# Kernel tuning notes

Hardware: AMD Instinct MI355X
Metric: run time of the kernel (lower is better)

Reference implementation:

```python
import jax, jax.numpy as jnp
import numpy as np
from jax import lax

# Dimensions (ModelArgs with d_model=1024)
B, L = 2, 1024
D_MODEL = 1024
D_INNER = 2048          # expand * d_model
D_STATE = 16
DT_RANK = 64            # ceil(d_model / 16)
D_CONV = 4


def setup_inputs() -> dict:
    key = jax.random.key(0)
    ks = jax.random.split(key, 8)
    sc = lambda k, shp, s: jax.random.normal(k, shp, dtype=jnp.float32) * s
    x = jax.random.normal(ks[0], (B, L, D_MODEL), dtype=jnp.float32)
    W_in = sc(ks[1], (2 * D_INNER, D_MODEL), 0.02)
    conv_w = sc(ks[2], (D_INNER, D_CONV), 0.2)
    conv_b = jnp.zeros((D_INNER,), jnp.float32)
    W_x = sc(ks[3], (DT_RANK + 2 * D_STATE, D_INNER), 0.02)
    dt_init_std = DT_RANK ** -0.5
    W_dt = jax.random.uniform(ks[4], (D_INNER, DT_RANK), jnp.float32,
                              -dt_init_std, dt_init_std)
    # dt_proj bias: inverse-softplus of dt ~ logUniform(dt_min, dt_max)
    dt_min, dt_max = 1e-3, 1e-1
    u = jax.random.uniform(ks[5], (D_INNER,), jnp.float32)
    dt = jnp.exp(u * (np.log(dt_max) - np.log(dt_min)) + np.log(dt_min))
    dt = jnp.clip(dt, 1e-4, None)
    b_dt = dt + jnp.log(-jnp.expm1(-dt))
    A_log = jnp.log(jnp.tile(jnp.arange(1, D_STATE + 1, dtype=jnp.float32)[None, :],
                             (D_INNER, 1)))
    D = jnp.ones((D_INNER,), jnp.float32)
    W_out = sc(ks[6], (D_MODEL, D_INNER), 0.02)
    return {"x": x, "W_in": W_in, "conv_w": conv_w, "conv_b": conv_b,
            "W_x": W_x, "W_dt": W_dt, "b_dt": b_dt, "A_log": A_log,
            "D": D, "W_out": W_out}


def reference(x, W_in, conv_w, conv_b, W_x, W_dt, b_dt, A_log, D, W_out):
    b, l, _ = x.shape
    d_in, n = A_log.shape
    k = conv_w.shape[1]

    # in_proj, split into conv branch and gating residual
    x_and_res = x @ W_in.T                                 # (b, l, 2*d_in)
    xz, res = jnp.split(x_and_res, [d_in], axis=-1)

    # Causal depthwise conv1d (kernel k, left-pad k-1, truncate to l)
    xp = jnp.pad(xz, ((0, 0), (k - 1, 0), (0, 0)))         # (b, l+k-1, d_in)
    xc = conv_b[None, None, :] + sum(
        xp[:, i:i + l, :] * conv_w[None, None, :, i] for i in range(k))
    xc = jax.nn.silu(xc)                                   # (b, l, d_in)

    # x_proj -> delta, B, C
    x_dbl = xc @ W_x.T                                     # (b, l, dt_rank+2n)
    dlt, Bm, Cm = jnp.split(x_dbl, [DT_RANK, DT_RANK + n], axis=-1)
    delta = jax.nn.softplus(dlt @ W_dt.T + b_dt)           # (b, l, d_in)

    # selective scan
    A = -jnp.exp(A_log)                                    # (d_in, n)
    dA = jnp.exp(delta[..., None] * A[None, None])         # (b, l, d_in, n)
    dBu = (delta * xc)[..., None] * Bm[:, :, None, :]      # (b, l, d_in, n)

    def step(h, inp):
        dA_t, dBu_t, C_t = inp                             # (b,d,n),(b,d,n),(b,n)
        h = dA_t * h + dBu_t
        y = jnp.einsum('bdn,bn->bd', h, C_t)
        return h, y

    h0 = jnp.zeros((b, d_in, n), xc.dtype)
    _, ys = lax.scan(step, h0, (dA.transpose(1, 0, 2, 3),
                                dBu.transpose(1, 0, 2, 3),
                                Cm.transpose(1, 0, 2)))
    y = ys.transpose(1, 0, 2) + xc * D[None, None, :]      # (b, l, d_in)

    y = y * jax.nn.silu(res)
    return y @ W_out.T                                     # (b, l, d_model)
```

## Files before the change

### kernel.cpp

```cpp
#include <hip/hip_runtime.h>
#include <hip/hip_bf16.h>
#include <cmath>

#define DEV __device__ __forceinline__

typedef float  f32x4  __attribute__((ext_vector_type(4)));
typedef __bf16 bf16x8 __attribute__((ext_vector_type(8)));
using u16 = unsigned short;

constexpr int CB   = 2;
constexpr int CLEN = 1024;
constexpr int CDM  = 1024;
constexpr int CDI  = 2048;
constexpr int CM   = CB * CLEN;
constexpr int NCHUNK = 64;
constexpr int CHL    = 16;

DEV u16 f2bf(float f) {
  unsigned u = __builtin_bit_cast(unsigned, f);
  unsigned r = (u + 0x7fffu + ((u >> 16) & 1u)) >> 16;
  return (u16)r;
}
DEV float bf2f(u16 v) { return __builtin_bit_cast(float, ((unsigned)v) << 16); }

DEV ushort4 f4bf(float4 v) {
  ushort4 o;
  o.x = f2bf(v.x); o.y = f2bf(v.y); o.z = f2bf(v.z); o.w = f2bf(v.w);
  return o;
}

constexpr int CG_X   = 524288;
constexpr int CG_WIN = CG_X   + 1048576;
constexpr int CG_WDT = CG_WIN + 32768;
constexpr int CG_WO  = CG_WDT + 524288;
constexpr int CG_WX  = CG_WO  + 65536;

__global__ void cast_all_k(const float* __restrict__ x, const float* __restrict__ W_in,
                           const float* __restrict__ W_dt, const float* __restrict__ W_out,
                           const float* __restrict__ W_x,
                           u16* __restrict__ xb, u16* __restrict__ W_inb,
                           u16* __restrict__ W_dtb, u16* __restrict__ W_outb,
                           u16* __restrict__ W_xb)
{
  int i = blockIdx.x * blockDim.x + threadIdx.x;
  if (i < CG_X) {
    reinterpret_cast<ushort4*>(xb)[i] = f4bf(reinterpret_cast<const float4*>(x)[i]);
  } else if (i < CG_WIN) {
    int j = i - CG_X;
    reinterpret_cast<ushort4*>(W_inb)[j] = f4bf(reinterpret_cast<const float4*>(W_in)[j]);
  } else if (i < CG_WDT) {
    int j = i - CG_WIN;
    reinterpret_cast<ushort4*>(W_dtb)[j] = f4bf(reinterpret_cast<const float4*>(W_dt)[j]);
  } else if (i < CG_WO) {
    int j = i - CG_WDT;
    reinterpret_cast<ushort4*>(W_outb)[j] = f4bf(reinterpret_cast<const float4*>(W_out)[j]);
  } else {
    int j = i - CG_WO;
    int base = j * 4, row = base >> 11, col = base & 2047;
    float4 v = make_float4(0.f, 0.f, 0.f, 0.f);
    if (row < 96) v = *reinterpret_cast<const float4*>(W_x + row * 2048 + col);
    reinterpret_cast<ushort4*>(W_xb)[j] = f4bf(v);
  }
}

DEV void gload_lds16(const void* g, void* l) {
  __builtin_amdgcn_global_load_lds(
      (const __attribute__((address_space(1))) void*)g,
      (__attribute__((address_space(3))) void*)l, 16, 0, 0);
}

template <int EPI, int SPLITK>
__global__ __launch_bounds__(256, 2)
void gemm_bt(const u16* __restrict__ A, const u16* __restrict__ Bw,
             float* __restrict__ C, u16* __restrict__ Cb,
             const float* __restrict__ bias,
             int Nd, int Kd, int lda, int ldb, int ldc, size_t slice_stride)
{
  __shared__ u16 As[128 * 32];
  __shared__ u16 Bs[128 * 32];
  const int tid  = threadIdx.x;
  const int wave = tid >> 6;
  const int lane = tid & 63;
  const int wm = wave >> 1, wn = wave & 1;
  const int row0 = blockIdx.y * 128;
  const int col0 = blockIdx.x * 128;
  const int lr = lane >> 2;
  const int lc = (lane & 3) * 8;

  const int kper = Kd / SPLITK;
  const int kbeg = (SPLITK > 1) ? blockIdx.z * kper : 0;
  float* Cz = (SPLITK > 1) ? C + (size_t)blockIdx.z * slice_stride : C;

  f32x4 acc[4][4] = {};

  for (int k0 = kbeg; k0 < kbeg + kper; k0 += 32) {
#pragma unroll
    for (int j = 0; j < 2; ++j) {
      const int rb = j * 64 + wave * 16;
      gload_lds16(A  + (size_t)(row0 + rb + lr) * lda + k0 + lc, As + rb * 32);
      gload_lds16(Bw + (size_t)(col0 + rb + lr) * ldb + k0 + lc, Bs + rb * 32);
    }
    __syncthreads();

    const int q  = lane >> 4;
    const int mr = lane & 15;
    bf16x8 af[4], bfr[4];
#pragma unroll
    for (int t = 0; t < 4; ++t) {
      af[t]  = *reinterpret_cast<const bf16x8*>(As + (wm * 64 + t * 16 + mr) * 32 + q * 8);
      bfr[t] = *reinterpret_cast<const bf16x8*>(Bs + (wn * 64 + t * 16 + mr) * 32 + q * 8);
    }
#pragma unroll
    for (int mt = 0; mt < 4; ++mt)
#pragma unroll
      for (int nt = 0; nt < 4; ++nt)
        acc[mt][nt] = __builtin_amdgcn_mfma_f32_16x16x32_bf16(af[mt], bfr[nt], acc[mt][nt], 0, 0, 0);
    __syncthreads();
  }

  const int q  = lane >> 4;
  const int cn = lane & 15;
#pragma unroll
  for (int mt = 0; mt < 4; ++mt)
#pragma unroll
    for (int nt = 0; nt < 4; ++nt)
#pragma unroll
      for (int r = 0; r < 4; ++r) {
        const int row = row0 + wm * 64 + mt * 16 + q * 4 + r;
        const int col = col0 + wn * 64 + nt * 16 + cn;
        float v = acc[mt][nt][r];
        if (EPI == 3) {
          v += bias[col];
          v = (v > 15.f) ? v : log1pf(__expf(v));
        }
        if (EPI == 0) Cz[(size_t)row * ldc + col] = v;
        else          Cb[(size_t)row * ldc + col] = f2bf(v);
      }
}

__global__ void xdbl_reduce_k(const float* __restrict__ part,
                              float* __restrict__ xdbl, u16* __restrict__ xdblb)
{
  int i = blockIdx.x * blockDim.x + threadIdx.x;
  float4 s = reinterpret_cast<const float4*>(part)[i];
#pragma unroll
  for (int z = 1; z < 8; ++z) {
    float4 p = reinterpret_cast<const float4*>(part + (size_t)z * CM * 128)[i];
    s.x += p.x; s.y += p.y; s.z += p.z; s.w += p.w;
  }
  reinterpret_cast<float4*>(xdbl)[i] = s;
  reinterpret_cast<ushort4*>(xdblb)[i] = f4bf(s);
}

__global__ void out_reduce_k(const float* __restrict__ part, float* __restrict__ out)
{
  int i = blockIdx.x * blockDim.x + threadIdx.x;
  float4 s = reinterpret_cast<const float4*>(part)[i];
#pragma unroll
  for (int z = 1; z < 4; ++z) {
    float4 p = reinterpret_cast<const float4*>(part + (size_t)z * CM * CDM)[i];
    s.x += p.x; s.y += p.y; s.z += p.z; s.w += p.w;
  }
  reinterpret_cast<float4*>(out)[i] = s;
}

__global__ void conv_silu_k(const u16* __restrict__ xzb, const float4* __restrict__ cw4,
                            const float* __restrict__ cb,
                            u16* __restrict__ xcb, u16* __restrict__ rsb)
{
  int idx = blockIdx.x * blockDim.x + threadIdx.x;
  int d   = idx & (CDI - 1);
  int row = idx >> 11;
  int l   = row & (CLEN - 1);
  float4 wv = cw4[d];
  const float* wp = (const float*)&wv;
  float acc = cb[d];
#pragma unroll
  for (int i = 0; i < 4; ++i) {
    int ls = l - 3 + i;
    float v = (ls >= 0) ? bf2f(xzb[(size_t)(row - l + ls) * 4096 + d]) : 0.f;
    acc += v * wp[i];
  }
  float s = acc / (1.f + __expf(-acc));
  xcb[idx] = f2bf(s);
  float r = bf2f(xzb[(size_t)row * 4096 + CDI + d]);
  rsb[idx] = f2bf(r / (1.f + __expf(-r)));
}

__global__ __launch_bounds__(256)
void scan_p1(const u16* __restrict__ delta_b, const u16* __restrict__ xcb,
             const float* __restrict__ xdbl, const float* __restrict__ A_log,
             float* __restrict__ P, float* __restrict__ S)
{
  __shared__ float sB[CHL * 16];
  const int t = threadIdx.x;
  const int d = blockIdx.x * 256 + t;
  const int c = blockIdx.y, b = blockIdx.z;

  if (t < CHL * 16) {
    int ll = t >> 4, n = t & 15;
    sB[t] = xdbl[(size_t)(b * CLEN + c * CHL + ll) * 128 + 64 + n];
  }
  __syncthreads();

  float An[16], Pv[16], Sv[16];
#pragma unroll
  for (int n = 0; n < 16; ++n) {
    An[n] = -__expf(A_log[d * 16 + n]);
    Pv[n] = 1.f; Sv[n] = 0.f;
  }
  const size_t rbase = (size_t)(b * CLEN + c * CHL) * CDI + d;
  for (int ll = 0; ll < CHL; ++ll) {
    float dl = bf2f(delta_b[rbase + (size_t)ll * CDI]);
    float u  = bf2f(xcb[rbase + (size_t)ll * CDI]);
    float du = dl * u;
#pragma unroll
    for (int n = 0; n < 16; ++n) {
      float a = __expf(dl * An[n]);
      Pv[n] *= a;
      Sv[n] = a * Sv[n] + du * sB[ll * 16 + n];
    }
  }
  const size_t o = (size_t)((b * NCHUNK + c) * 16) * CDI + d;
#pragma unroll
  for (int n = 0; n < 16; ++n) {
    P[o + (size_t)n * CDI] = Pv[n];
    S[o + (size_t)n * CDI] = Sv[n];
  }
}

__global__ void scan_p2(const float* __restrict__ P, const float* __restrict__ S,
                        float* __restrict__ Hin)
{
  const int t = threadIdx.x;
  const int d = blockIdx.x * 256 + t;
  const int n = blockIdx.y, b = blockIdx.z;
  float h = 0.f;
#pragma unroll 8
  for (int c = 0; c < NCHUNK; ++c) {
    size_t o = (size_t)((b * NCHUNK + c) * 16 + n) * CDI + d;
    Hin[o] = h;
    h = P[o] * h + S[o];
  }
}

__global__ __launch_bounds__(256)
void scan_p3(const u16* __restrict__ delta_b, const u16* __restrict__ xcb,
             const float* __restrict__ xdbl, const float* __restrict__ A_log,
             const float* __restrict__ Dvec, const u16* __restrict__ rsb,
             const float* __restrict__ Hin, u16* __restrict__ ybarb)
{
  __shared__ float sB[CHL * 16];
  __shared__ float sC[CHL * 16];
  const int t = threadIdx.x;
  const int d = blockIdx.x * 256 + t;
  const int c = blockIdx.y, b = blockIdx.z;

  if (t < CHL * 16) {
    int ll = t >> 4, n = t & 15;
    size_t ro = (size_t)(b * CLEN + c * CHL + ll) * 128;
    sB[t] = xdbl[ro + 64 + n];
    sC[t] = xdbl[ro + 80 + n];
  }
  __syncthreads();

  float An[16], h[16];
  const size_t ho = (size_t)((b * NCHUNK + c) * 16) * CDI + d;
#pragma unroll
  for (int n = 0; n < 16; ++n) {
    An[n] = -__expf(A_log[d * 16 + n]);
    h[n]  = Hin[ho + (size_t)n * CDI];
  }
  const float Dd = Dvec[d];
  const size_t rbase = (size_t)(b * CLEN + c * CHL);
  for (int ll = 0; ll < CHL; ++ll) {
    size_t e = (rbase + ll) * CDI + d;
    float dl = bf2f(delta_b[e]);
    float u  = bf2f(xcb[e]);
    float du = dl * u;
    float y  = 0.f;
#pragma unroll
    for (int n = 0; n < 16; ++n) {
      float a = __expf(dl * An[n]);
      h[n] = a * h[n] + du * sB[ll * 16 + n];
      y += h[n] * sC[ll * 16 + n];
    }
    y += u * Dd;
    ybarb[e] = f2bf(y * bf2f(rsb[e]));
  }
}

extern "C" void kernel_launch(void* const* d_in, const int* in_sizes, int n_in,
                              void* d_out, int out_size, void* d_ws, size_t ws_size,
                              hipStream_t stream)
{
  (void)in_sizes; (void)n_in; (void)out_size; (void)ws_size;
  const float* x      = (const float*)d_in[0];
  const float* W_in   = (const float*)d_in[1];
  const float* conv_w = (const float*)d_in[2];
  const float* conv_b = (const float*)d_in[3];
  const float* W_x    = (const float*)d_in[4];
  const float* W_dt   = (const float*)d_in[5];
  const float* b_dt   = (const float*)d_in[6];
  const float* A_log  = (const float*)d_in[7];
  const float* Dvec   = (const float*)d_in[8];
  const float* W_out  = (const float*)d_in[9];
  float* out = (float*)d_out;

  constexpr size_t MB = 1048576;
  char* w = (char*)d_ws;
  u16*   xzres_b = (u16*)(w + 0);
  u16*   xb      = (u16*)(w + 16 * MB);
  u16*   W_inb   = (u16*)(w + 20 * MB);
  float* xpart   = (float*)(w + 28 * MB);
  float* opart   = (float*)(w + 0);
  float* Pb      = (float*)(w + 36 * MB);
  float* Sb      = (float*)(w + 52 * MB);
  float* Hin     = (float*)(w + 68 * MB);
  u16*   xcb     = (u16*)(w + 84 * MB);
  u16*   rsb     = (u16*)(w + 92 * MB);
  float* xdbl    = (float*)(w + 100 * MB);
  u16*   xdblb   = (u16*)(w + 101 * MB);
  u16*   W_xb    = (u16*)(w + 101 * MB + 512 * 1024);
  u16*   W_dtb   = (u16*)(w + 102 * MB);
  u16*   delta_b = (u16*)(w + 102 * MB + 256 * 1024);
  u16*   ybarb   = (u16*)(w + 110 * MB + 256 * 1024);
  u16*   W_outb  = (u16*)(w + 118 * MB + 256 * 1024);

  dim3 blk(256);
  cast_all_k<<<CG_WX / 256, blk, 0, stream>>>(x, W_in, W_dt, W_out, W_x,
                                              xb, W_inb, W_dtb, W_outb, W_xb);
  gemm_bt<1, 1><<<dim3(32, 16), blk, 0, stream>>>(xb, W_inb, nullptr, xzres_b, nullptr,
                                                  4096, 1024, 1024, 1024, 4096, 0);
  conv_silu_k<<<(CB * CLEN * CDI) / 256, blk, 0, stream>>>(xzres_b, (const float4*)conv_w,
                                                           conv_b, xcb, rsb);
  gemm_bt<0, 8><<<dim3(1, 16, 8), blk, 0, stream>>>(xcb, W_xb, xpart, nullptr, nullptr,
                                                    128, 2048, 2048, 2048, 128,
                                                    (size_t)CM * 128);
  xdbl_reduce_k<<<(CM * 128 / 4) / 256, blk, 0, stream>>>(xpart, xdbl, xdblb);
  gemm_bt<3, 1><<<dim3(16, 16), blk, 0, stream>>>(xdblb, W_dtb, nullptr, delta_b, b_dt,
                                                  2048, 64, 128, 64, 2048, 0);
  scan_p1<<<dim3(8, NCHUNK, 2), blk, 0, stream>>>(delta_b, xcb, xdbl, A_log, Pb, Sb);
  scan_p2<<<dim3(8, 16, 2), blk, 0, stream>>>(Pb, Sb, Hin);
  scan_p3<<<dim3(8, NCHUNK, 2), blk, 0, stream>>>(delta_b, xcb, xdbl, A_log, Dvec, rsb,
                                                  Hin, ybarb);
  gemm_bt<0, 4><<<dim3(8, 16, 4), blk, 0, stream>>>(ybarb, W_outb, opart, nullptr, nullptr,
                                                    1024, 2048, 2048, 2048, 1024,
                                                    (size_t)CM * CDM);
  out_reduce_k<<<(CM * CDM / 4) / 256, blk, 0, stream>>>(opart, out);
}
```

Measured before the change: 254.1 us.

## Register-prefetch GEMM tiles, fuse gate SiLU into scan, retune chunks and split-K

The GEMM drops direct global-to-LDS loads and instead prefetches the next K tile into registers while MFMAs run on the current LDS tile. The gate SiLU moves from the conv kernel into scan_p3, which removes the rsb buffer and its extra write and read. The scan now uses 32 chunks of length 32 instead of 64 of length 16, and the x_proj GEMM uses split-K 16, which means a larger reduction. The workspace layout is repacked so opart no longer aliases xzres_b, since scan_p3 now reads xzres_b.

```diff
diff --git a/kernel.cpp b/kernel.cpp
--- a/kernel.cpp
+++ b/kernel.cpp
@@ -13,8 +13,8 @@
 constexpr int CDM  = 1024;
 constexpr int CDI  = 2048;
 constexpr int CM   = CB * CLEN;
-constexpr int NCHUNK = 64;
-constexpr int CHL    = 16;
+constexpr int NCHUNK = 32;
+constexpr int CHL    = 32;
 
 DEV u16 f2bf(float f) {
   unsigned u = __builtin_bit_cast(unsigned, f);
@@ -63,12 +63,6 @@
   }
 }
 
-DEV void gload_lds16(const void* g, void* l) {
-  __builtin_amdgcn_global_load_lds(
-      (const __attribute__((address_space(1))) void*)g,
-      (__attribute__((address_space(3))) void*)l, 16, 0, 0);
-}
-
 template <int EPI, int SPLITK>
 __global__ __launch_bounds__(256, 2)
 void gemm_bt(const u16* __restrict__ A, const u16* __restrict__ Bw,
@@ -89,21 +83,38 @@
 
   const int kper = Kd / SPLITK;
   const int kbeg = (SPLITK > 1) ? blockIdx.z * kper : 0;
+  const int kend = kbeg + kper;
   float* Cz = (SPLITK > 1) ? C + (size_t)blockIdx.z * slice_stride : C;
 
+  const u16* Ag = A  + (size_t)(row0 + wave * 16 + lr) * lda + lc;
+  const u16* Bg = Bw + (size_t)(col0 + wave * 16 + lr) * ldb + lc;
+  u16* Al0 = As + (wave * 16 + lr) * 32 + lc;
+  u16* Al1 = As + (64 + wave * 16 + lr) * 32 + lc;
+  u16* Bl0 = Bs + (wave * 16 + lr) * 32 + lc;
+  u16* Bl1 = Bs + (64 + wave * 16 + lr) * 32 + lc;
+
+  bf16x8 pa0 = *reinterpret_cast<const bf16x8*>(Ag + kbeg);
+  bf16x8 pa1 = *reinterpret_cast<const bf16x8*>(Ag + (size_t)64 * lda + kbeg);
+  bf16x8 pb0 = *reinterpret_cast<const bf16x8*>(Bg + kbeg);
+  bf16x8 pb1 = *reinterpret_cast<const bf16x8*>(Bg + (size_t)64 * ldb + kbeg);
+
   f32x4 acc[4][4] = {};
-
-  for (int k0 = kbeg; k0 < kbeg + kper; k0 += 32) {
-#pragma unroll
-    for (int j = 0; j < 2; ++j) {
-      const int rb = j * 64 + wave * 16;
-      gload_lds16(A  + (size_t)(row0 + rb + lr) * lda + k0 + lc, As + rb * 32);
-      gload_lds16(Bw + (size_t)(col0 + rb + lr) * ldb + k0 + lc, Bs + rb * 32);
-    }
+  const int q  = lane >> 4;
+  const int mr = lane & 15;
+
+  for (int k0 = kbeg; k0 < kend; k0 += 32) {
     __syncthreads();
-
-    const int q  = lane >> 4;
-    const int mr = lane & 15;
+    *reinterpret_cast<bf16x8*>(Al0) = pa0;
+    *reinterpret_cast<bf16x8*>(Al1) = pa1;
+    *reinterpret_cast<bf16x8*>(Bl0) = pb0;
+    *reinterpret_cast<bf16x8*>(Bl1) = pb1;
+    __syncthreads();
+    const int k1 = (k0 + 32 < kend) ? k0 + 32 : kbeg;
+    pa0 = *reinterpret_cast<const bf16x8*>(Ag + k1);
+    pa1 = *reinterpret_cast<const bf16x8*>(Ag + (size_t)64 * lda + k1);
+    pb0 = *reinterpret_cast<const bf16x8*>(Bg + k1);
+    pb1 = *reinterpret_cast<const bf16x8*>(Bg + (size_t)64 * ldb + k1);
+
     bf16x8 af[4], bfr[4];
 #pragma unroll
     for (int t = 0; t < 4; ++t) {
@@ -115,10 +126,8 @@
 #pragma unroll
       for (int nt = 0; nt < 4; ++nt)
         acc[mt][nt] = __builtin_amdgcn_mfma_f32_16x16x32_bf16(af[mt], bfr[nt], acc[mt][nt], 0, 0, 0);
-    __syncthreads();
-  }
-
-  const int q  = lane >> 4;
+  }
+
   const int cn = lane & 15;
 #pragma unroll
   for (int mt = 0; mt < 4; ++mt)
@@ -144,7 +153,7 @@
   int i = blockIdx.x * blockDim.x + threadIdx.x;
   float4 s = reinterpret_cast<const float4*>(part)[i];
 #pragma unroll
-  for (int z = 1; z < 8; ++z) {
+  for (int z = 1; z < 16; ++z) {
     float4 p = reinterpret_cast<const float4*>(part + (size_t)z * CM * 128)[i];
     s.x += p.x; s.y += p.y; s.z += p.z; s.w += p.w;
   }
@@ -165,8 +174,7 @@
 }
 
 __global__ void conv_silu_k(const u16* __restrict__ xzb, const float4* __restrict__ cw4,
-                            const float* __restrict__ cb,
-                            u16* __restrict__ xcb, u16* __restrict__ rsb)
+                            const float* __restrict__ cb, u16* __restrict__ xcb)
 {
   int idx = blockIdx.x * blockDim.x + threadIdx.x;
   int d   = idx & (CDI - 1);
@@ -183,8 +191,6 @@
   }
   float s = acc / (1.f + __expf(-acc));
   xcb[idx] = f2bf(s);
-  float r = bf2f(xzb[(size_t)row * 4096 + CDI + d]);
-  rsb[idx] = f2bf(r / (1.f + __expf(-r)));
 }
 
 __global__ __launch_bounds__(256)
@@ -197,9 +203,9 @@
   const int d = blockIdx.x * 256 + t;
   const int c = blockIdx.y, b = blockIdx.z;
 
-  if (t < CHL * 16) {
-    int ll = t >> 4, n = t & 15;
-    sB[t] = xdbl[(size_t)(b * CLEN + c * CHL + ll) * 128 + 64 + n];
+  for (int i = t; i < CHL * 16; i += 256) {
+    int ll = i >> 4, n = i & 15;
+    sB[i] = xdbl[(size_t)(b * CLEN + c * CHL + ll) * 128 + 64 + n];
   }
   __syncthreads();
 
@@ -247,7 +253,7 @@
 __global__ __launch_bounds__(256)
 void scan_p3(const u16* __restrict__ delta_b, const u16* __restrict__ xcb,
              const float* __restrict__ xdbl, const float* __restrict__ A_log,
-             const float* __restrict__ Dvec, const u16* __restrict__ rsb,
+             const float* __restrict__ Dvec, const u16* __restrict__ xzb,
              const float* __restrict__ Hin, u16* __restrict__ ybarb)
 {
   __shared__ float sB[CHL * 16];
@@ -256,11 +262,11 @@
   const int d = blockIdx.x * 256 + t;
   const int c = blockIdx.y, b = blockIdx.z;
 
-  if (t < CHL * 16) {
-    int ll = t >> 4, n = t & 15;
+  for (int i = t; i < CHL * 16; i += 256) {
+    int ll = i >> 4, n = i & 15;
     size_t ro = (size_t)(b * CLEN + c * CHL + ll) * 128;
-    sB[t] = xdbl[ro + 64 + n];
-    sC[t] = xdbl[ro + 80 + n];
+    sB[i] = xdbl[ro + 64 + n];
+    sC[i] = xdbl[ro + 80 + n];
   }
   __syncthreads();
 
@@ -286,7 +292,9 @@
       y += h[n] * sC[ll * 16 + n];
     }
     y += u * Dd;
-    ybarb[e] = f2bf(y * bf2f(rsb[e]));
+    float r = bf2f(xzb[(rbase + ll) * 4096 + CDI + d]);
+    float sr = r / (1.f + __expf(-r));
+    ybarb[e] = f2bf(y * sr);
   }
 }
 
@@ -312,20 +320,19 @@
   u16*   xzres_b = (u16*)(w + 0);
   u16*   xb      = (u16*)(w + 16 * MB);
   u16*   W_inb   = (u16*)(w + 20 * MB);
-  float* xpart   = (float*)(w + 28 * MB);
-  float* opart   = (float*)(w + 0);
-  float* Pb      = (float*)(w + 36 * MB);
-  float* Sb      = (float*)(w + 52 * MB);
-  float* Hin     = (float*)(w + 68 * MB);
-  u16*   xcb     = (u16*)(w + 84 * MB);
-  u16*   rsb     = (u16*)(w + 92 * MB);
-  float* xdbl    = (float*)(w + 100 * MB);
-  u16*   xdblb   = (u16*)(w + 101 * MB);
-  u16*   W_xb    = (u16*)(w + 101 * MB + 512 * 1024);
-  u16*   W_dtb   = (u16*)(w + 102 * MB);
-  u16*   delta_b = (u16*)(w + 102 * MB + 256 * 1024);
-  u16*   ybarb   = (u16*)(w + 110 * MB + 256 * 1024);
-  u16*   W_outb  = (u16*)(w + 118 * MB + 256 * 1024);
+  u16*   xcb     = (u16*)(w + 28 * MB);
+  u16*   delta_b = (u16*)(w + 36 * MB);
+  float* xpart   = (float*)(w + 44 * MB);
+  float* xdbl    = (float*)(w + 60 * MB);
+  u16*   xdblb   = (u16*)(w + 61 * MB);
+  u16*   W_xb    = (u16*)(w + 61 * MB + 512 * 1024);
+  u16*   W_dtb   = (u16*)(w + 62 * MB);
+  float* Pb      = (float*)(w + 63 * MB);
+  float* Sb      = (float*)(w + 71 * MB);
+  float* Hin     = (float*)(w + 79 * MB);
+  u16*   ybarb   = (u16*)(w + 87 * MB);
+  u16*   W_outb  = (u16*)(w + 95 * MB);
+  float* opart   = (float*)(w + 99 * MB);
 
   dim3 blk(256);
   cast_all_k<<<CG_WX / 256, blk, 0, stream>>>(x, W_in, W_dt, W_out, W_x,
@@ -333,17 +340,17 @@
   gemm_bt<1, 1><<<dim3(32, 16), blk, 0, stream>>>(xb, W_inb, nullptr, xzres_b, nullptr,
                                                   4096, 1024, 1024, 1024, 4096, 0);
   conv_silu_k<<<(CB * CLEN * CDI) / 256, blk, 0, stream>>>(xzres_b, (const float4*)conv_w,
-                                                           conv_b, xcb, rsb);
-  gemm_bt<0, 8><<<dim3(1, 16, 8), blk, 0, stream>>>(xcb, W_xb, xpart, nullptr, nullptr,
-                                                    128, 2048, 2048, 2048, 128,
-                                                    (size_t)CM * 128);
+                                                           conv_b, xcb);
+  gemm_bt<0, 16><<<dim3(1, 16, 16), blk, 0, stream>>>(xcb, W_xb, xpart, nullptr, nullptr,
+                                                      128, 2048, 2048, 2048, 128,
+                                                      (size_t)CM * 128);
   xdbl_reduce_k<<<(CM * 128 / 4) / 256, blk, 0, stream>>>(xpart, xdbl, xdblb);
   gemm_bt<3, 1><<<dim3(16, 16), blk, 0, stream>>>(xdblb, W_dtb, nullptr, delta_b, b_dt,
                                                   2048, 64, 128, 64, 2048, 0);
   scan_p1<<<dim3(8, NCHUNK, 2), blk, 0, stream>>>(delta_b, xcb, xdbl, A_log, Pb, Sb);
   scan_p2<<<dim3(8, 16, 2), blk, 0, stream>>>(Pb, Sb, Hin);
-  scan_p3<<<dim3(8, NCHUNK, 2), blk, 0, stream>>>(delta_b, xcb, xdbl, A_log, Dvec, rsb,
-                                                  Hin, ybarb);
+  scan_p3<<<dim3(8, NCHUNK, 2), blk, 0, stream>>>(delta_b, xcb, xdbl, A_log, Dvec,
+                                                  xzres_b, Hin, ybarb);
   gemm_bt<0, 4><<<dim3(8, 16, 4), blk, 0, stream>>>(ybarb, W_outb, opart, nullptr, nullptr,
                                                     1024, 2048, 2048, 2048, 1024,
                                                     (size_t)CM * CDM);
```

After: 250.6 us. About the same (-1.4%).
